# Kernel optimization log

Hardware: AMD Instinct MI355X
Metric: run time of the kernel (lower is better)

## Reference

```python
import jax, jax.numpy as jnp
import numpy as np

SIZE = 65536
MAX_EDGES = 16777216  # n_edges = min(0.1*SIZE^2, MAX_EDGES) = MAX_EDGES, so all edges active


def setup_inputs() -> dict:
    key = jax.random.key(0)
    k1, k2, k3, k4 = jax.random.split(key, 4)
    x = jax.random.normal(k1, (SIZE,), dtype=jnp.float32)
    edge_weights = jax.random.normal(k2, (MAX_EDGES,), dtype=jnp.float32) * (2.0 / SIZE) ** 0.5
    bias = jnp.zeros((SIZE,), dtype=jnp.float32)
    src = jax.random.randint(k3, (MAX_EDGES,), 0, SIZE, dtype=jnp.int64 if jax.config.jax_enable_x64 else jnp.int32)
    dst = jax.random.randint(k4, (MAX_EDGES,), 0, SIZE, dtype=jnp.int64 if jax.config.jax_enable_x64 else jnp.int32)
    return {"x": x, "edge_weights": edge_weights, "bias": bias, "src": src, "dst": dst}


def reference(x, edge_weights, bias, src, dst):
    # gather -> elementwise multiply -> scatter_add -> + bias
    weighted = x[src] * edge_weights                    # [E]
    out = jax.ops.segment_sum(weighted, dst, num_segments=SIZE)  # [size]
    return out + bias
```

## Files before the change

### kernel.cpp

```cpp
#include <hip/hip_runtime.h>


#define NNODES  65536
#define NEDGES  16777216
#define RANGES  2
#define BINS    (NNODES / RANGES)
#define THREADS 1024
#define NCOPIES 128
#define GROUPS  16
#define CPG     (NCOPIES / GROUPS)

__global__ __launch_bounds__(THREADS, 4) void hist_kernel(
    const float* __restrict__ x,
    const float* __restrict__ w,
    const int*   __restrict__ src,
    const int*   __restrict__ dst,
    float*       __restrict__ ws,
    int B)
{
    extern __shared__ float h[];

    const int b  = blockIdx.x;
    const int r  = b & (RANGES - 1);
    const int c  = b >> 1;
    const int lo = r * BINS;

    for (int i = threadIdx.x; i < BINS; i += THREADS) h[i] = 0.0f;
    __syncthreads();

    const int4*   src4 = (const int4*)src;
    const int4*   dst4 = (const int4*)dst;
    const float4* wgt4 = (const float4*)w;

    const int n8 = NEDGES / 8;
    for (int g = c * THREADS + (int)threadIdx.x; g < n8; g += B * THREADS) {
        int4   sa = src4[2 * g], sb = src4[2 * g + 1];
        int4   da = dst4[2 * g], db = dst4[2 * g + 1];
        float4 wa = wgt4[2 * g], wb = wgt4[2 * g + 1];

        int      s[8]  = { sa.x, sa.y, sa.z, sa.w, sb.x, sb.y, sb.z, sb.w };
        unsigned bin[8] = {
            (unsigned)(da.x - lo), (unsigned)(da.y - lo),
            (unsigned)(da.z - lo), (unsigned)(da.w - lo),
            (unsigned)(db.x - lo), (unsigned)(db.y - lo),
            (unsigned)(db.z - lo), (unsigned)(db.w - lo) };
        float    wv[8] = { wa.x, wa.y, wa.z, wa.w, wb.x, wb.y, wb.z, wb.w };

        float v[8];
        #pragma unroll
        for (int k = 0; k < 8; ++k) {
            v[k] = 0.0f;
            if (bin[k] < (unsigned)BINS) v[k] = x[s[k]] * wv[k];
        }
        #pragma unroll
        for (int k = 0; k < 8; ++k) {
            if (bin[k] < (unsigned)BINS) atomicAdd(&h[bin[k]], v[k]);
        }
    }
    __syncthreads();

    float* outc = ws + (size_t)c * NNODES + lo;
    for (int i = threadIdx.x; i < BINS; i += THREADS) outc[i] = h[i];
}

__global__ __launch_bounds__(256) void reduceA_kernel(float* __restrict__ ws)
{
    const int NB = NNODES / (256 * 4);
    int g  = blockIdx.x / NB;
    int jb = blockIdx.x % NB;
    int i4 = jb * 256 + (int)threadIdx.x;

    float4* w4 = (float4*)ws;
    const int stride4 = NNODES / 4;

    float4 acc = w4[(size_t)(g * CPG) * stride4 + i4];
    #pragma unroll
    for (int cc = 1; cc < CPG; ++cc) {
        float4 t = w4[(size_t)(g * CPG + cc) * stride4 + i4];
        acc.x += t.x; acc.y += t.y; acc.z += t.z; acc.w += t.w;
    }
    w4[(size_t)(g * CPG) * stride4 + i4] = acc;
}

__global__ __launch_bounds__(256) void reduceB_kernel(
    const float* __restrict__ ws,
    const float* __restrict__ bias,
    float*       __restrict__ out)
{
    int i4 = blockIdx.x * 256 + (int)threadIdx.x;
    const float4* w4 = (const float4*)ws;
    const int stride4 = NNODES / 4;

    float4 acc = ((const float4*)bias)[i4];
    #pragma unroll
    for (int g = 0; g < GROUPS; ++g) {
        float4 t = w4[(size_t)(g * CPG) * stride4 + i4];
        acc.x += t.x; acc.y += t.y; acc.z += t.z; acc.w += t.w;
    }
    ((float4*)out)[i4] = acc;
}

__global__ __launch_bounds__(256) void reduce_generic_kernel(
    const float* __restrict__ ws,
    const float* __restrict__ bias,
    float*       __restrict__ out,
    int B)
{
    int i = blockIdx.x * 256 + (int)threadIdx.x;
    float acc = bias[i];
    for (int cc = 0; cc < B; ++cc) acc += ws[(size_t)cc * NNODES + i];
    out[i] = acc;
}

__global__ __launch_bounds__(256) void init_out_kernel(
    const float* __restrict__ bias, float* __restrict__ out)
{
    int i = blockIdx.x * blockDim.x + threadIdx.x;
    if (i < NNODES) out[i] = bias[i];
}

__global__ __launch_bounds__(256) void edge_atomic_kernel(
    const float* __restrict__ x, const float* __restrict__ w,
    const int* __restrict__ src, const int* __restrict__ dst,
    float* __restrict__ out)
{
    const int n4 = NEDGES / 4;
    int tid = blockIdx.x * blockDim.x + threadIdx.x;
    int stride = gridDim.x * blockDim.x;
    for (int i = tid; i < n4; i += stride) {
        int4 s = ((const int4*)src)[i];
        int4 d = ((const int4*)dst)[i];
        float4 ww = ((const float4*)w)[i];
        atomicAdd(&out[d.x], x[s.x] * ww.x);
        atomicAdd(&out[d.y], x[s.y] * ww.y);
        atomicAdd(&out[d.z], x[s.z] * ww.z);
        atomicAdd(&out[d.w], x[s.w] * ww.w);
    }
}

extern "C" void kernel_launch(void* const* d_in, const int* in_sizes, int n_in,
                              void* d_out, int out_size, void* d_ws, size_t ws_size,
                              hipStream_t stream) {
    const float* x    = (const float*)d_in[0];
    const float* w    = (const float*)d_in[1];
    const float* bias = (const float*)d_in[2];
    const int*   src  = (const int*)d_in[3];
    const int*   dst  = (const int*)d_in[4];
    float* out = (float*)d_out;
    float* ws  = (float*)d_ws;

    size_t copies = ws_size / ((size_t)NNODES * sizeof(float));
    int B = (int)(copies < NCOPIES ? copies : NCOPIES);

    if (B >= 1) {
        hist_kernel<<<B * RANGES, THREADS, BINS * sizeof(float), stream>>>(
            x, w, src, dst, ws, B);
        if (B == NCOPIES) {
            reduceA_kernel<<<GROUPS * (NNODES / 1024), 256, 0, stream>>>(ws);
            reduceB_kernel<<<NNODES / 1024, 256, 0, stream>>>(ws, bias, out);
        } else {
            reduce_generic_kernel<<<NNODES / 256, 256, 0, stream>>>(ws, bias, out, B);
        }
    } else {
        init_out_kernel<<<NNODES / 256, 256, 0, stream>>>(bias, out);
        edge_atomic_kernel<<<4096, 256, 0, stream>>>(x, w, src, dst, out);
    }
}
```

Measured before the change: 272.7 us.

## Software-pipeline edge loads and x gathers ahead of shared-memory atomics

Restructures the histogram loop into a three-stage software pipeline. Edge indices and weights are prefetched two iterations ahead and the x gathers one iteration ahead, while LDS atomics run for the current iteration. Out-of-range edges now do a gather from x[0] and an atomic add of zero to a masked bin instead of being skipped by branches. The shared-to-global copy also uses float4 stores. The aim is to hide global-load latency behind LDS atomic work, at the cost of more registers and some wasted gathers and atomics.

```diff
diff --git a/kernel.cpp b/kernel.cpp
--- a/kernel.cpp
+++ b/kernel.cpp
@@ -10,6 +10,46 @@
 #define GROUPS  16
 #define CPG     (NCOPIES / GROUPS)
 
+struct EQ { int4 sa, sb, da, db; float4 wa, wb; };
+
+__device__ __forceinline__ EQ load_eq(const int4* __restrict__ s4,
+                                      const int4* __restrict__ d4,
+                                      const float4* __restrict__ w4, int g) {
+    EQ e;
+    e.sa = s4[2 * g];     e.sb = s4[2 * g + 1];
+    e.da = d4[2 * g];     e.db = d4[2 * g + 1];
+    e.wa = w4[2 * g];     e.wb = w4[2 * g + 1];
+    return e;
+}
+
+struct Frag { unsigned bin[8]; float xv[8]; float wv[8]; };
+
+__device__ __forceinline__ void issue_gather(const float* __restrict__ x,
+                                             const EQ& e, int lo, Frag& f) {
+    const int s[8] = { e.sa.x, e.sa.y, e.sa.z, e.sa.w,
+                       e.sb.x, e.sb.y, e.sb.z, e.sb.w };
+    const int d[8] = { e.da.x, e.da.y, e.da.z, e.da.w,
+                       e.db.x, e.db.y, e.db.z, e.db.w };
+    const float wv[8] = { e.wa.x, e.wa.y, e.wa.z, e.wa.w,
+                          e.wb.x, e.wb.y, e.wb.z, e.wb.w };
+    #pragma unroll
+    for (int k = 0; k < 8; ++k) {
+        unsigned bin = (unsigned)(d[k] - lo);
+        unsigned idx = (bin < (unsigned)BINS) ? (unsigned)s[k] : 0u;
+        f.bin[k] = bin;
+        f.xv[k]  = x[idx];
+        f.wv[k]  = wv[k];
+    }
+}
+
+__device__ __forceinline__ void ds_pass(float* h, const Frag& f) {
+    #pragma unroll
+    for (int k = 0; k < 8; ++k) {
+        float val = (f.bin[k] < (unsigned)BINS) ? f.xv[k] * f.wv[k] : 0.0f;
+        atomicAdd(&h[f.bin[k] & (BINS - 1)], val);
+    }
+}
+
 __global__ __launch_bounds__(THREADS, 4) void hist_kernel(
     const float* __restrict__ x,
     const float* __restrict__ w,
@@ -32,35 +72,39 @@
     const int4*   dst4 = (const int4*)dst;
     const float4* wgt4 = (const float4*)w;
 
-    const int n8 = NEDGES / 8;
-    for (int g = c * THREADS + (int)threadIdx.x; g < n8; g += B * THREADS) {
-        int4   sa = src4[2 * g], sb = src4[2 * g + 1];
-        int4   da = dst4[2 * g], db = dst4[2 * g + 1];
-        float4 wa = wgt4[2 * g], wb = wgt4[2 * g + 1];
-
-        int      s[8]  = { sa.x, sa.y, sa.z, sa.w, sb.x, sb.y, sb.z, sb.w };
-        unsigned bin[8] = {
-            (unsigned)(da.x - lo), (unsigned)(da.y - lo),
-            (unsigned)(da.z - lo), (unsigned)(da.w - lo),
-            (unsigned)(db.x - lo), (unsigned)(db.y - lo),
-            (unsigned)(db.z - lo), (unsigned)(db.w - lo) };
-        float    wv[8] = { wa.x, wa.y, wa.z, wa.w, wb.x, wb.y, wb.z, wb.w };
-
-        float v[8];
-        #pragma unroll
-        for (int k = 0; k < 8; ++k) {
-            v[k] = 0.0f;
-            if (bin[k] < (unsigned)BINS) v[k] = x[s[k]] * wv[k];
+    const int n8      = NEDGES / 8;
+    const int gstride = B * THREADS;
+    const int iters   = n8 / gstride;
+    int g = c * THREADS + (int)threadIdx.x;
+
+    if (iters * gstride == n8 && iters >= 3) {
+        EQ e0 = load_eq(src4, dst4, wgt4, g);
+        EQ e1 = load_eq(src4, dst4, wgt4, g + gstride);
+        Frag f0;
+        issue_gather(x, e0, lo, f0);
+
+        for (int i = 0; i + 1 < iters; ++i) {
+            int gl = (i + 2 < iters) ? (g + 2 * gstride) : g;
+            EQ e2 = load_eq(src4, dst4, wgt4, gl);
+            Frag f1;
+            issue_gather(x, e1, lo, f1);
+            ds_pass(h, f0);
+            f0 = f1; e1 = e2; g += gstride;
         }
-        #pragma unroll
-        for (int k = 0; k < 8; ++k) {
-            if (bin[k] < (unsigned)BINS) atomicAdd(&h[bin[k]], v[k]);
+        ds_pass(h, f0);
+    } else {
+        for (int gg = g; gg < n8; gg += gstride) {
+            EQ e = load_eq(src4, dst4, wgt4, gg);
+            Frag f;
+            issue_gather(x, e, lo, f);
+            ds_pass(h, f);
         }
     }
     __syncthreads();
 
-    float* outc = ws + (size_t)c * NNODES + lo;
-    for (int i = threadIdx.x; i < BINS; i += THREADS) outc[i] = h[i];
+    float4* outc4 = (float4*)(ws + (size_t)c * NNODES + lo);
+    const float4* h4 = (const float4*)h;
+    for (int i = threadIdx.x; i < BINS / 4; i += THREADS) outc4[i] = h4[i];
 }
 
 __global__ __launch_bounds__(256) void reduceA_kernel(float* __restrict__ ws)
```

Measured after the change: 323.8 us. 1.19x slower.
